# Kernel optimization log

Hardware: AMD Instinct MI355X
Metric: run time of the kernel (lower is better)

The kernel has to match this reference:

```python
import jax, jax.numpy as jnp
import numpy as np

K = 20          # knn neighbors (init kwarg k)
LEAK = 0.2      # LeakyReLU negative slope
EPS = 1e-5      # BatchNorm eps


def knn(x, k):
    # x: (B, D, N) -> indices (B, N, K) of k nearest (largest negative sq-dist)
    inner = -2.0 * jnp.einsum('bin,bim->bnm', x, x)
    xx = jnp.sum(x * x, axis=1, keepdims=True)            # (B,1,N)
    pd = -xx - inner - jnp.swapaxes(xx, 1, 2)             # (B,N,N)
    return jax.lax.top_k(pd, k)[1]


def gather_graph_feature(x, idx):
    # x: (B,D,N), idx: (B,N,K) -> (B, 2D, N, K)
    feat = jax.vmap(lambda xb, ib: xb[:, ib])(x, idx)     # (B,D,N,K)
    xc = x[..., None]                                     # (B,D,N,1)
    return jnp.concatenate([feat - xc, jnp.broadcast_to(xc, feat.shape)], axis=1)


def bn_lrelu(y, g, b, axes):
    mu = jnp.mean(y, axis=axes, keepdims=True)
    var = jnp.var(y, axis=axes, keepdims=True)            # biased var (torch BN train)
    shape = [1] * y.ndim
    shape[1] = -1
    y = (y - mu) * jax.lax.rsqrt(var + EPS) * g.reshape(shape) + b.reshape(shape)
    return jnp.where(y >= 0, y, LEAK * y)


def edge_block(x, idx, w, g, b):
    f = gather_graph_feature(x, idx)                      # (B,2D,N,K)
    y = jnp.einsum('oc,bcnk->bonk', w, f)                 # 1x1 Conv2d, no bias
    y = bn_lrelu(y, g, b, (0, 2, 3))
    return jnp.max(y, axis=-1)                            # max over K -> (B,O,N)


def setup_inputs() -> dict:
    key = jax.random.key(0)
    ks = jax.random.split(key, 8)
    B, D, N = 2, 2, 4096
    out_dim = 512
    pts = jax.random.normal(ks[0], (B, D, N), dtype=jnp.float32)
    dims = [(64, 4), (64, 128), (128, 128), (256, 256), (out_dim, 512)]
    inp = {'pts': pts}
    for i, (o, c) in enumerate(dims):
        inp[f'w{i+1}'] = jax.random.normal(ks[i + 1], (o, c), dtype=jnp.float32) * 0.05
        inp[f'g{i+1}'] = jnp.ones((o,), dtype=jnp.float32)
        inp[f'b{i+1}'] = jnp.zeros((o,), dtype=jnp.float32)
    return inp


def reference(pts, w1, g1, b1, w2, g2, b2, w3, g3, b3, w4, g4, b4, w5, g5, b5):
    idx = knn(pts, K)
    x1 = edge_block(pts, idx, w1, g1, b1)   # (B,64,N)
    x2 = edge_block(x1, idx, w2, g2, b2)    # (B,64,N)
    x3 = edge_block(x2, idx, w3, g3, b3)    # (B,128,N)
    x4 = edge_block(x3, idx, w4, g4, b4)    # (B,256,N)
    x = jnp.concatenate([x1, x2, x3, x4], axis=1)         # (B,512,N)
    y = jnp.einsum('oc,bcn->bon', w5, x)                  # 1x1 Conv1d, no bias
    return bn_lrelu(y, g5, b5, (0, 2))
```

## Files before the change

### kernel.cpp

```cpp
#include <hip/hip_runtime.h>
#include <hip/hip_bf16.h>
#include <math.h>

#define BB 2
#define NN 4096
#define PP (BB*NN)
#define KK 20
#define LEAK 0.2f
#define EPSB 1e-5f

typedef short sv8 __attribute__((ext_vector_type(8)));
typedef float f4  __attribute__((ext_vector_type(4)));

__device__ inline unsigned short f2bf(float f) {
    unsigned u = __float_as_uint(f);
    unsigned r = (u + 0x7FFFu + ((u >> 16) & 1u)) >> 16;
    return (unsigned short)r;
}
__device__ inline float bf2f(unsigned short h) {
    return __uint_as_float((unsigned)h << 16);
}
__device__ inline void gload16(const void* g, void* l) {
    __builtin_amdgcn_global_load_lds(
        (const __attribute__((address_space(1))) unsigned int*)g,
        (__attribute__((address_space(3))) unsigned int*)l, 16, 0, 0);
}

__global__ __launch_bounds__(256) void knn_kernel(const float* __restrict__ pts,
                                                  int* __restrict__ idx,
                                                  float* __restrict__ pts_t) {
    __shared__ unsigned int hist[256];
    __shared__ unsigned int scanres[3];
    __shared__ unsigned int cnt2[2];
    __shared__ unsigned long long blist[512];

    int r = blockIdx.x;
    int b = r >> 12, n = r & (NN - 1);
    const float* X0 = pts + (size_t)b * 2 * NN;
    const float* X1 = X0 + NN;
    int tid = threadIdx.x;
    float x0n = X0[n], x1n = X1[n];
    if (tid == 0) {
        pts_t[(size_t)r * 2 + 0] = x0n;
        pts_t[(size_t)r * 2 + 1] = x1n;
    }
    float xxn = __fadd_rn(__fmul_rn(x0n, x0n), __fmul_rn(x1n, x1n));
    float negxxn = __fsub_rn(0.f, xxn);

    float pdv[16];
    #pragma unroll
    for (int q = 0; q < 16; ++q) {
        int m = q * 256 + tid;
        float x0m = X0[m], x1m = X1[m];
        float xxm = __fadd_rn(__fmul_rn(x0m, x0m), __fmul_rn(x1m, x1m));
        float dot = __builtin_fmaf(x1n, x1m, __fmul_rn(x0n, x0m));
        float inner = __fmul_rn(-2.f, dot);
        float t1 = __fsub_rn(negxxn, inner);
        pdv[q] = __fsub_rn(t1, xxm);
    }

    int shift = 24;
    for (int attempt = 0; attempt < 3; ++attempt) {
        hist[tid] = 0;
        __syncthreads();
        float scale = (float)(1u << shift);
        #pragma unroll
        for (int q = 0; q < 16; ++q) {
            float s = fmaxf(-pdv[q], 0.f);
            unsigned int ki = (unsigned int)fminf(s * scale, 4.294e9f);
            unsigned int bin = ki >> 16;
            if (bin < 255u) atomicAdd(&hist[bin], 1u);
        }
        __syncthreads();
        if (tid < 64) {
            uint4 hv = *(const uint4*)&hist[tid * 4];
            unsigned int p0 = hv.x, p1 = p0 + hv.y, p2 = p1 + hv.z, p3 = p2 + hv.w;
            unsigned int lanesum = p3, inc = p3;
            #pragma unroll
            for (int s2 = 1; s2 < 64; s2 <<= 1) {
                unsigned int o = __shfl_up(inc, s2, 64);
                if (tid >= s2) inc += o;
            }
            unsigned int excl = inc - lanesum;
            bool flag = (inc >= KK);
            unsigned long long bal = __ballot(flag);
            int firstlane = (bal == 0ULL) ? -1 : (__ffsll((long long)bal) - 1);
            if (tid == 0) scanres[0] = (bal != 0ULL) ? 1u : 0u;
            if (tid == firstlane) {
                unsigned int c0 = excl + p0, c1 = excl + p1, c2 = excl + p2;
                int t = (c0 >= KK) ? 0 : (c1 >= KK) ? 1 : (c2 >= KK) ? 2 : 3;
                unsigned int cumb = (t == 0) ? excl : (t == 1) ? c0 : (t == 2) ? c1 : c2;
                scanres[1] = (unsigned)(tid * 4 + t);
                scanres[2] = cumb;
            }
        }
        __syncthreads();
        if (scanres[0]) break;
        shift -= 6;
        __syncthreads();
    }

    unsigned int bstar = scanres[1];
    unsigned int cumb  = scanres[2];
    if (tid == 0) { cnt2[0] = 0; cnt2[1] = 0; }
    __syncthreads();

    float scale = (float)(1u << shift);
    #pragma unroll
    for (int q = 0; q < 16; ++q) {
        float s = fmaxf(-pdv[q], 0.f);
        unsigned int ki = (unsigned int)fminf(s * scale, 4.294e9f);
        unsigned int bin = ki >> 16;
        if (bin > 255u) bin = 255u;
        int m = q * 256 + tid;
        if (bin < bstar) {
            unsigned int slot = atomicAdd(&cnt2[0], 1u);
            idx[(size_t)r * KK + slot] = m;
        } else if (bin == bstar) {
            unsigned int pos = atomicAdd(&cnt2[1], 1u);
            if (pos < 512u) {
                unsigned int ub = __float_as_uint(pdv[q]);
                unsigned int fk = (ub & 0x80000000u) ? ~ub : (ub | 0x80000000u);
                blist[pos] = ((unsigned long long)(~fk) << 32) | (unsigned int)m;
            }
        }
    }
    __syncthreads();

    int need = KK - (int)cumb;
    int L = (int)min(cnt2[1], 512u);
    if (tid < 64) {
        unsigned long long e[8];
        #pragma unroll
        for (int i = 0; i < 8; ++i) {
            int p = tid + 64 * i;
            e[i] = (p < L) ? blist[p] : ~0ULL;
        }
        unsigned long long lmin = e[0];
        #pragma unroll
        for (int i = 1; i < 8; ++i) lmin = (e[i] < lmin) ? e[i] : lmin;
        for (int p = 0; p < need; ++p) {
            unsigned long long gm = lmin;
            #pragma unroll
            for (int s2 = 32; s2 > 0; s2 >>= 1) {
                unsigned long long o = __shfl_xor(gm, s2, 64);
                if (o < gm) gm = o;
            }
            if (lmin == gm) {
                #pragma unroll
                for (int i = 0; i < 8; ++i) if (e[i] == gm) e[i] = ~0ULL;
                lmin = e[0];
                #pragma unroll
                for (int i = 1; i < 8; ++i) lmin = (e[i] < lmin) ? e[i] : lmin;
                idx[(size_t)r * KK + cumb + p] = (int)(gm & 0xFFFFFFFFu);
            }
        }
    }
}

__global__ __launch_bounds__(256) void proj_gemm(const float* __restrict__ X, int ldx, int C,
                                                 const float* __restrict__ W, int O, int mode,
                                                 float* __restrict__ outU, float* __restrict__ outV) {
    __shared__ float Xs[16][65];
    __shared__ float Ws[16][65];
    int row0 = blockIdx.x * 64, col0 = blockIdx.y * 64;
    int tid = threadIdx.x;
    int tx = tid % 16, ty = tid / 16;
    float acc[4][4] = {};
    for (int c0 = 0; c0 < C; c0 += 16) {
        for (int i = 0; i < 4; ++i) {
            int mm = ty + i * 16;
            float val = 0.f;
            if (c0 + tx < C) val = X[(size_t)(row0 + mm) * ldx + c0 + tx];
            Xs[tx][mm] = val;
        }
        for (int i = 0; i < 4; ++i) {
            int jj = ty + i * 16;
            int j = col0 + jj;
            float val = 0.f;
            if (c0 + tx < C) {
                if (mode == 0) {
                    if (j < O) val = W[(size_t)j * (2 * C) + c0 + tx];
                    else {
                        const float* wr = W + (size_t)(j - O) * (2 * C);
                        val = wr[C + c0 + tx] - wr[c0 + tx];
                    }
                } else {
                    val = W[(size_t)j * C + c0 + tx];
                }
            }
            Ws[tx][jj] = val;
        }
        __syncthreads();
        int kmax = (C - c0 < 16) ? (C - c0) : 16;
        for (int kk = 0; kk < kmax; ++kk) {
            float a[4], bw[4];
            #pragma unroll
            for (int i = 0; i < 4; ++i) a[i] = Xs[kk][ty * 4 + i];
            #pragma unroll
            for (int j = 0; j < 4; ++j) bw[j] = Ws[kk][tx * 4 + j];
            #pragma unroll
            for (int i = 0; i < 4; ++i)
                #pragma unroll
                for (int j = 0; j < 4; ++j)
                    acc[i][j] = fmaf(a[i], bw[j], acc[i][j]);
        }
        __syncthreads();
    }
    for (int i = 0; i < 4; ++i) {
        int rr = row0 + ty * 4 + i;
        for (int j = 0; j < 4; ++j) {
            int jg = col0 + tx * 4 + j;
            float vv = acc[i][j];
            if (mode == 0) {
                if (jg < O) outU[(size_t)rr * O + jg] = vv;
                else        outV[(size_t)rr * O + (jg - O)] = vv;
            } else {
                outU[(size_t)rr * O + jg] = vv;
            }
        }
    }
}

__global__ __launch_bounds__(256) void convert_all(const float* __restrict__ w2,
                                                   const float* __restrict__ w3,
                                                   const float* __restrict__ w4,
                                                   const float* __restrict__ w5,
                                                   unsigned short* __restrict__ bh,
                                                   unsigned short* __restrict__ bl) {
    int i = blockIdx.x * 256 + threadIdx.x;
    if (i >= 352256) return;
    const float* w; int O, C, mode, base;
    if (i < 8192)       { w = w2; O = 64;  C = 64;  mode = 0; base = 0; }
    else if (i < 24576) { w = w3; O = 128; C = 64;  mode = 0; base = 8192; }
    else if (i < 90112) { w = w4; O = 256; C = 128; mode = 0; base = 24576; }
    else                { w = w5; O = 512; C = 512; mode = 1; base = 90112; }
    int j = i - base;
    int row = j / C, c = j - row * C;
    float v;
    if (mode == 0) {
        if (row < O) v = w[(size_t)row * 2 * C + c];
        else {
            const float* wr = w + (size_t)(row - O) * 2 * C;
            v = wr[C + c] - wr[c];
        }
    } else {
        v = w[(size_t)row * C + c];
    }
    unsigned short h = f2bf(v);
    bh[i] = h;
    bl[i] = f2bf(v - bf2f(h));
}

__global__ __launch_bounds__(256) void mfma_gemm64(const unsigned short* __restrict__ Xh,
                                                   const unsigned short* __restrict__ Xl,
                                                   int ldx, int K,
                                                   const unsigned short* __restrict__ Bh,
                                                   const unsigned short* __restrict__ Bl,
                                                   int O,
                                                   float* __restrict__ outU,
                                                   float* __restrict__ outV) {
    __shared__ unsigned short Ah[256 * 8], Al[256 * 8], Bhs[256 * 8], Bls[256 * 8];
    int row0 = blockIdx.x * 64, col0 = blockIdx.y * 64;
    int tid = threadIdx.x;
    int wid = tid >> 6, lane = tid & 63;
    int wm = wid & 1, wn = wid >> 1;
    int l15 = lane & 15, l4 = lane >> 4;
    int m = tid & 63, kb = tid >> 6;

    f4 acc[2][2];
    #pragma unroll
    for (int i = 0; i < 2; ++i)
        #pragma unroll
        for (int j = 0; j < 2; ++j) { acc[i][j][0]=0.f; acc[i][j][1]=0.f; acc[i][j][2]=0.f; acc[i][j][3]=0.f; }

    for (int k0 = 0; k0 < K; k0 += 32) {
        size_t ga = (size_t)(row0 + m) * ldx + k0 + kb * 8;
        size_t gb = (size_t)(col0 + m) * K + k0 + kb * 8;
        gload16(Xh + ga, &Ah[(size_t)(wid * 64) * 8]);
        gload16(Xl + ga, &Al[(size_t)(wid * 64) * 8]);
        gload16(Bh + gb, &Bhs[(size_t)(wid * 64) * 8]);
        gload16(Bl + gb, &Bls[(size_t)(wid * 64) * 8]);
        __syncthreads();

        sv8 bhf[2], blf[2];
        #pragma unroll
        for (int fn = 0; fn < 2; ++fn) {
            int nn2 = wn * 32 + fn * 16 + l15;
            bhf[fn] = *(const sv8*)&Bhs[(size_t)(l4 * 64 + nn2) * 8];
            blf[fn] = *(const sv8*)&Bls[(size_t)(l4 * 64 + nn2) * 8];
        }
        #pragma unroll
        for (int fm = 0; fm < 2; ++fm) {
            int mm = wm * 32 + fm * 16 + l15;
            sv8 ah = *(const sv8*)&Ah[(size_t)(l4 * 64 + mm) * 8];
            sv8 al = *(const sv8*)&Al[(size_t)(l4 * 64 + mm) * 8];
            #pragma unroll
            for (int fn = 0; fn < 2; ++fn) {
                acc[fm][fn] = __builtin_amdgcn_mfma_f32_16x16x32_bf16(ah, bhf[fn], acc[fm][fn], 0, 0, 0);
                acc[fm][fn] = __builtin_amdgcn_mfma_f32_16x16x32_bf16(ah, blf[fn], acc[fm][fn], 0, 0, 0);
                acc[fm][fn] = __builtin_amdgcn_mfma_f32_16x16x32_bf16(al, bhf[fn], acc[fm][fn], 0, 0, 0);
            }
        }
        __syncthreads();
    }

    #pragma unroll
    for (int fm = 0; fm < 2; ++fm) {
        int rbase = row0 + wm * 32 + fm * 16 + l4 * 4;
        #pragma unroll
        for (int fn = 0; fn < 2; ++fn) {
            int jg = col0 + wn * 32 + fn * 16 + l15;
            #pragma unroll
            for (int e = 0; e < 4; ++e) {
                float vv = acc[fm][fn][e];
                int p = rbase + e;
                if (jg < O) outU[(size_t)p * O + jg] = vv;
                else        outV[(size_t)p * O + (jg - O)] = vv;
            }
        }
    }
}

__global__ __launch_bounds__(256) void mfma_gemm128s(const unsigned short* __restrict__ Xh,
                                                     int ldx, int K,
                                                     const unsigned short* __restrict__ Bh,
                                                     int O,
                                                     float* __restrict__ outU) {
    __shared__ unsigned short Ah[512 * 8], Bhs[512 * 8];
    int row0 = blockIdx.x * 128, col0 = blockIdx.y * 128;
    int tid = threadIdx.x;
    int wid = tid >> 6, lane = tid & 63;
    int wm = wid & 1, wn = wid >> 1;
    int l15 = lane & 15, l4 = lane >> 4;

    f4 acc[4][4];
    #pragma unroll
    for (int i = 0; i < 4; ++i)
        #pragma unroll
        for (int j = 0; j < 4; ++j) { acc[i][j][0]=0.f; acc[i][j][1]=0.f; acc[i][j][2]=0.f; acc[i][j][3]=0.f; }

    for (int k0 = 0; k0 < K; k0 += 32) {
        #pragma unroll
        for (int j = 0; j < 2; ++j) {
            int c = tid + 256 * j;
            int m = c & 127, kb = c >> 7;
            size_t ga = (size_t)(row0 + m) * ldx + k0 + kb * 8;
            size_t gb = (size_t)(col0 + m) * K + k0 + kb * 8;
            gload16(Xh + ga, &Ah[(size_t)(wid * 64 + 256 * j) * 8]);
            gload16(Bh + gb, &Bhs[(size_t)(wid * 64 + 256 * j) * 8]);
        }
        __syncthreads();

        sv8 bhf[4];
        #pragma unroll
        for (int fn = 0; fn < 4; ++fn) {
            int nn2 = wn * 64 + fn * 16 + l15;
            bhf[fn] = *(const sv8*)&Bhs[(size_t)(l4 * 128 + nn2) * 8];
        }
        #pragma unroll
        for (int fm = 0; fm < 4; ++fm) {
            int mm = wm * 64 + fm * 16 + l15;
            sv8 ah = *(const sv8*)&Ah[(size_t)(l4 * 128 + mm) * 8];
            #pragma unroll
            for (int fn = 0; fn < 4; ++fn)
                acc[fm][fn] = __builtin_amdgcn_mfma_f32_16x16x32_bf16(ah, bhf[fn], acc[fm][fn], 0, 0, 0);
        }
        __syncthreads();
    }

    #pragma unroll
    for (int fm = 0; fm < 4; ++fm) {
        int rbase = row0 + wm * 64 + fm * 16 + l4 * 4;
        #pragma unroll
        for (int fn = 0; fn < 4; ++fn) {
            int jg = col0 + wn * 64 + fn * 16 + l15;
            #pragma unroll
            for (int e = 0; e < 4; ++e)
                outU[(size_t)(rbase + e) * O + jg] = acc[fm][fn][e];
        }
    }
}

__global__ __launch_bounds__(256) void edge_stats(const float* __restrict__ u,
                                                  const float* __restrict__ v,
                                                  const int* __restrict__ idx,
                                                  int O, int PPL,
                                                  float* __restrict__ mx, float* __restrict__ mn,
                                                  float* __restrict__ partial) {
    __shared__ float red[4 * 256];
    int tid = threadIdx.x;
    int CH2 = O >> 1;
    int PS = 256 / CH2;
    int co = tid % CH2;
    int ps = tid / CH2;
    float s1a = 0.f, s1b = 0.f, s2a = 0.f, s2b = 0.f;
    for (int pi = 0; pi < PPL; ++pi) {
        int r = (blockIdx.x * PS + ps) * PPL + pi;
        int b = r >> 12;
        const float* ub = u + (size_t)b * NN * O + 2 * co;
        float2 vv = *(const float2*)&v[(size_t)r * O + 2 * co];
        const int* ip = idx + (size_t)r * KK;
        int mreg[KK];
        #pragma unroll
        for (int k = 0; k < KK; ++k) mreg[k] = ip[k];
        float2 uv[KK];
        #pragma unroll
        for (int k = 0; k < KK; ++k) uv[k] = *(const float2*)&ub[(size_t)mreg[k] * O];
        float bxa = -INFINITY, bxb = -INFINITY, bna = INFINITY, bnb = INFINITY;
        #pragma unroll
        for (int k = 0; k < KK; ++k) {
            float y0 = uv[k].x + vv.x, y1 = uv[k].y + vv.y;
            s1a += y0; s2a = fmaf(y0, y0, s2a);
            s1b += y1; s2b = fmaf(y1, y1, s2b);
            bxa = fmaxf(bxa, y0); bna = fminf(bna, y0);
            bxb = fmaxf(bxb, y1); bnb = fminf(bnb, y1);
        }
        *(float2*)&mx[(size_t)r * O + 2 * co] = make_float2(bxa, bxb);
        *(float2*)&mn[(size_t)r * O + 2 * co] = make_float2(bna, bnb);
    }
    red[0 * 256 + tid] = s1a;
    red[1 * 256 + tid] = s1b;
    red[2 * 256 + tid] = s2a;
    red[3 * 256 + tid] = s2b;
    __syncthreads();
    for (int s = PS >> 1; s > 0; s >>= 1) {
        if (ps < s) {
            int oth = tid + s * CH2;
            red[0 * 256 + tid] += red[0 * 256 + oth];
            red[1 * 256 + tid] += red[1 * 256 + oth];
            red[2 * 256 + tid] += red[2 * 256 + oth];
            red[3 * 256 + tid] += red[3 * 256 + oth];
        }
        __syncthreads();
    }
    if (ps == 0) {
        size_t base = (size_t)blockIdx.x * 2 * O;
        partial[base + 2 * co]         = red[0 * 256 + tid];
        partial[base + 2 * co + 1]     = red[1 * 256 + tid];
        partial[base + O + 2 * co]     = red[2 * 256 + tid];
        partial[base + O + 2 * co + 1] = red[3 * 256 + tid];
    }
}

__global__ __launch_bounds__(256) void stats_reduce(const float* __restrict__ partial, int nblk,
                                                    int O, float cnt,
                                                    const float* __restrict__ g,
                                                    const float* __restrict__ bsh,
                                                    float* __restrict__ st) {
    __shared__ float r1[4], r2[4];
    int o = blockIdx.x, tid = threadIdx.x;
    float s1 = 0.f, s2 = 0.f;
    for (int bk = tid; bk < nblk; bk += 256) {
        size_t base = (size_t)bk * 2 * O;
        s1 += partial[base + o];
        s2 += partial[base + O + o];
    }
    #pragma unroll
    for (int s = 32; s > 0; s >>= 1) {
        s1 += __shfl_down(s1, s, 64);
        s2 += __shfl_down(s2, s, 64);
    }
    if ((tid & 63) == 0) { r1[tid >> 6] = s1; r2[tid >> 6] = s2; }
    __syncthreads();
    if (tid == 0) {
        s1 = r1[0] + r1[1] + r1[2] + r1[3];
        s2 = r2[0] + r2[1] + r2[2] + r2[3];
        float mu = s1 / cnt;
        float var = s2 / cnt - mu * mu;
        float x = var + EPSB;
        float rr = rsqrtf(x);
        rr = rr * (1.5f - 0.5f * x * rr * rr);
        float sc = g[o] * rr;
        st[o] = sc;
        st[O + o] = bsh[o] - mu * sc;
    }
}

__global__ void apply_edge(const float* __restrict__ mx, const float* __restrict__ mn,
                           const float* __restrict__ st, int O, int choff,
                           unsigned short* __restrict__ xh, unsigned short* __restrict__ xl,
                           int writelo) {
    int e2 = blockIdx.x * 256 + threadIdx.x;
    int half = O >> 1;
    if (e2 >= PP * half) return;
    int r = e2 / half, o = (e2 - r * half) * 2;
    float2 sc = *(const float2*)&st[o];
    float2 tt = *(const float2*)&st[O + o];
    float2 vx = *(const float2*)&mx[(size_t)r * O + o];
    float2 vn = *(const float2*)&mn[(size_t)r * O + o];
    float b0 = (sc.x >= 0.f) ? vx.x : vn.x;
    float b1 = (sc.y >= 0.f) ? vx.y : vn.y;
    float y0 = fmaf(sc.x, b0, tt.x); y0 = (y0 >= 0.f) ? y0 : LEAK * y0;
    float y1 = fmaf(sc.y, b1, tt.y); y1 = (y1 >= 0.f) ? y1 : LEAK * y1;
    unsigned short h0 = f2bf(y0), h1 = f2bf(y1);
    size_t d = (size_t)r * 512 + choff + o;
    ((unsigned int*)xh)[d >> 1] = (unsigned int)h0 | ((unsigned int)h1 << 16);
    if (writelo) {
        unsigned short l0 = f2bf(y0 - bf2f(h0)), l1 = f2bf(y1 - bf2f(h1));
        ((unsigned int*)xl)[d >> 1] = (unsigned int)l0 | ((unsigned int)l1 << 16);
    }
}

__global__ __launch_bounds__(256) void final_stats(const float* __restrict__ y5,
                                                   float* __restrict__ partial) {
    int blk = blockIdx.x, t = threadIdx.x;
    float s1a = 0.f, s2a = 0.f, s1b = 0.f, s2b = 0.f;
    for (int rr = 0; rr < 128; ++rr) {
        size_t row = (size_t)(blk * 128 + rr) * 512;
        float va = y5[row + t], vb = y5[row + t + 256];
        s1a += va; s2a = fmaf(va, va, s2a);
        s1b += vb; s2b = fmaf(vb, vb, s2b);
    }
    partial[((size_t)blk * 512 + t) * 2 + 0] = s1a;
    partial[((size_t)blk * 512 + t) * 2 + 1] = s2a;
    partial[((size_t)blk * 512 + t + 256) * 2 + 0] = s1b;
    partial[((size_t)blk * 512 + t + 256) * 2 + 1] = s2b;
}

__global__ __launch_bounds__(64) void final_reduce(const float* __restrict__ partial, int nblk,
                                                   float cnt,
                                                   const float* __restrict__ g,
                                                   const float* __restrict__ bsh,
                                                   float* __restrict__ st) {
    int c = blockIdx.x, tid = threadIdx.x;
    float s1 = 0.f, s2 = 0.f;
    for (int bk = tid; bk < nblk; bk += 64) {
        size_t base = ((size_t)bk * 512 + c) * 2;
        s1 += partial[base];
        s2 += partial[base + 1];
    }
    #pragma unroll
    for (int s = 32; s > 0; s >>= 1) {
        s1 += __shfl_down(s1, s, 64);
        s2 += __shfl_down(s2, s, 64);
    }
    if (tid == 0) {
        float mu = s1 / cnt;
        float var = s2 / cnt - mu * mu;
        float x = var + EPSB;
        float rr = rsqrtf(x);
        rr = rr * (1.5f - 0.5f * x * rr * rr);
        float sc = g[c] * rr;
        st[c] = sc;
        st[512 + c] = bsh[c] - mu * sc;
    }
}

__global__ __launch_bounds__(256) void final_apply(const float* __restrict__ y5,
                                                   const float* __restrict__ st,
                                                   float* __restrict__ out) {
    __shared__ float tile[32][33];
    int n0 = blockIdx.x * 32, o0 = blockIdx.y * 32, b = blockIdx.z;
    int tx = threadIdx.x, ty = threadIdx.y;
    for (int i = 0; i < 4; ++i) {
        int nl = ty + i * 8;
        tile[nl][tx] = y5[((size_t)(b * NN + n0 + nl)) * 512 + o0 + tx];
    }
    __syncthreads();
    for (int i = 0; i < 4; ++i) {
        int ol = ty + i * 8;
        int o = o0 + ol;
        float sc = st[o], tt = st[512 + o];
        float yv = fmaf(sc, tile[tx][ol], tt);
        yv = (yv >= 0.f) ? yv : LEAK * yv;
        out[((size_t)b * 512 + o) * NN + n0 + tx] = yv;
    }
}

extern "C" void kernel_launch(void* const* d_in, const int* in_sizes, int n_in,
                              void* d_out, int out_size, void* d_ws, size_t ws_size,
                              hipStream_t stream) {
    const float* pts = (const float*)d_in[0];
    const float* w[5]; const float* g[5]; const float* bsh[5];
    for (int i = 0; i < 5; ++i) {
        w[i]   = (const float*)d_in[1 + 3 * i];
        g[i]   = (const float*)d_in[2 + 3 * i];
        bsh[i] = (const float*)d_in[3 + 3 * i];
    }
    float* out = (float*)d_out;

    unsigned short* xh = (unsigned short*)d_ws;
    unsigned short* xl = xh + (size_t)PP * 512;
    float* u    = (float*)(xl + (size_t)PP * 512);
    float* v    = u    + (size_t)PP * 256;
    float* mxb  = v    + (size_t)PP * 256;
    float* mnb  = mxb  + (size_t)PP * 256;
    float* y5   = u;
    float* ptst = mnb  + (size_t)PP * 256;
    int*   idxb = (int*)(ptst + (size_t)PP * 2);
    float* part = (float*)(idxb + (size_t)PP * KK);
    float* st   = part + (size_t)1048576;
    unsigned short* wh_all = (unsigned short*)(st + 1024);
    unsigned short* wl_all = wh_all + 352256;

    knn_kernel<<<PP, 256, 0, stream>>>(pts, idxb, ptst);
    convert_all<<<1376, 256, 0, stream>>>(w[1], w[2], w[3], w[4], wh_all, wl_all);

    const int Cs[4]    = {2, 64, 64, 128};
    const int Os[4]    = {64, 64, 128, 256};
    const int choffs[4]= {0, 64, 128, 256};
    const int inoffs[4]= {0, 0, 64, 128};
    const int woffs[4] = {0, 0, 8192, 24576};

    for (int li = 0; li < 4; ++li) {
        int C = Cs[li], O = Os[li];
        if (li == 0) {
            dim3 gg(PP / 64, (2 * O) / 64);
            proj_gemm<<<gg, 256, 0, stream>>>(ptst, 2, C, w[0], O, 0, u, v);
        } else {
            dim3 gg(PP / 64, (2 * O) / 64);
            mfma_gemm64<<<gg, 256, 0, stream>>>(xh + inoffs[li], xl + inoffs[li], 512, C,
                                                wh_all + woffs[li], wl_all + woffs[li], O, u, v);
        }
        int PS  = 512 / O;
        int PPL = (O == 256) ? 2 : 1;
        int nblk = PP / (PS * PPL);
        edge_stats<<<nblk, 256, 0, stream>>>(u, v, idxb, O, PPL, mxb, mnb, part);
        stats_reduce<<<O, 256, 0, stream>>>(part, nblk, O, (float)((size_t)PP * KK),
                                            g[li], bsh[li], st);
        apply_edge<<<(PP * O / 2 + 255) / 256, 256, 0, stream>>>(
            mxb, mnb, st, O, choffs[li], xh, xl, (li == 3) ? 0 : 1);
    }

    dim3 gf(PP / 128, 512 / 128);
    mfma_gemm128s<<<gf, 256, 0, stream>>>(xh, 512, 512, wh_all + 90112, 512, y5);
    final_stats<<<64, 256, 0, stream>>>(y5, part);
    final_reduce<<<512, 64, 0, stream>>>(part, 64, (float)PP, g[4], bsh[4], st);
    final_apply<<<dim3(NN / 32, 512 / 32, BB), dim3(32, 8), 0, stream>>>(y5, st, out);
}
```

Before: 194.0 us.

## Fuse final BN stats into GEMM epilogue, specialize layer-1 projection, cache kNN bins

The final GEMM now reduces per-column sum and sum of squares in its epilogue and writes one partial per row block, so the separate final_stats pass over y5 goes away and final_reduce reads 64 partials directly. The generic tiled proj_gemm for layer 1 is replaced by an elementwise kernel that reads points directly, which also drops the transposed points copy from the kNN kernel. The kNN kernel keeps its computed bin indices in registers instead of recomputing them in the selection pass, at the cost of extra register pressure.

```diff
diff --git a/kernel.cpp b/kernel.cpp
--- a/kernel.cpp
+++ b/kernel.cpp
@@ -27,8 +27,7 @@
 }
 
 __global__ __launch_bounds__(256) void knn_kernel(const float* __restrict__ pts,
-                                                  int* __restrict__ idx,
-                                                  float* __restrict__ pts_t) {
+                                                  int* __restrict__ idx) {
     __shared__ unsigned int hist[256];
     __shared__ unsigned int scanres[3];
     __shared__ unsigned int cnt2[2];
@@ -40,10 +39,6 @@
     const float* X1 = X0 + NN;
     int tid = threadIdx.x;
     float x0n = X0[n], x1n = X1[n];
-    if (tid == 0) {
-        pts_t[(size_t)r * 2 + 0] = x0n;
-        pts_t[(size_t)r * 2 + 1] = x1n;
-    }
     float xxn = __fadd_rn(__fmul_rn(x0n, x0n), __fmul_rn(x1n, x1n));
     float negxxn = __fsub_rn(0.f, xxn);
 
@@ -59,6 +54,7 @@
         pdv[q] = __fsub_rn(t1, xxm);
     }
 
+    int bins[16];
     int shift = 24;
     for (int attempt = 0; attempt < 3; ++attempt) {
         hist[tid] = 0;
@@ -69,6 +65,8 @@
             float s = fmaxf(-pdv[q], 0.f);
             unsigned int ki = (unsigned int)fminf(s * scale, 4.294e9f);
             unsigned int bin = ki >> 16;
+            if (bin > 255u) bin = 255u;
+            bins[q] = (int)bin;
             if (bin < 255u) atomicAdd(&hist[bin], 1u);
         }
         __syncthreads();
@@ -100,18 +98,14 @@
         __syncthreads();
     }
 
-    unsigned int bstar = scanres[1];
-    unsigned int cumb  = scanres[2];
+    int bstar = (int)scanres[1];
+    unsigned int cumb = scanres[2];
     if (tid == 0) { cnt2[0] = 0; cnt2[1] = 0; }
     __syncthreads();
 
-    float scale = (float)(1u << shift);
     #pragma unroll
     for (int q = 0; q < 16; ++q) {
-        float s = fmaxf(-pdv[q], 0.f);
-        unsigned int ki = (unsigned int)fminf(s * scale, 4.294e9f);
-        unsigned int bin = ki >> 16;
-        if (bin > 255u) bin = 255u;
+        int bin = bins[q];
         int m = q * 256 + tid;
         if (bin < bstar) {
             unsigned int slot = atomicAdd(&cnt2[0], 1u);
@@ -158,68 +152,18 @@
     }
 }
 
-__global__ __launch_bounds__(256) void proj_gemm(const float* __restrict__ X, int ldx, int C,
-                                                 const float* __restrict__ W, int O, int mode,
-                                                 float* __restrict__ outU, float* __restrict__ outV) {
-    __shared__ float Xs[16][65];
-    __shared__ float Ws[16][65];
-    int row0 = blockIdx.x * 64, col0 = blockIdx.y * 64;
-    int tid = threadIdx.x;
-    int tx = tid % 16, ty = tid / 16;
-    float acc[4][4] = {};
-    for (int c0 = 0; c0 < C; c0 += 16) {
-        for (int i = 0; i < 4; ++i) {
-            int mm = ty + i * 16;
-            float val = 0.f;
-            if (c0 + tx < C) val = X[(size_t)(row0 + mm) * ldx + c0 + tx];
-            Xs[tx][mm] = val;
-        }
-        for (int i = 0; i < 4; ++i) {
-            int jj = ty + i * 16;
-            int j = col0 + jj;
-            float val = 0.f;
-            if (c0 + tx < C) {
-                if (mode == 0) {
-                    if (j < O) val = W[(size_t)j * (2 * C) + c0 + tx];
-                    else {
-                        const float* wr = W + (size_t)(j - O) * (2 * C);
-                        val = wr[C + c0 + tx] - wr[c0 + tx];
-                    }
-                } else {
-                    val = W[(size_t)j * C + c0 + tx];
-                }
-            }
-            Ws[tx][jj] = val;
-        }
-        __syncthreads();
-        int kmax = (C - c0 < 16) ? (C - c0) : 16;
-        for (int kk = 0; kk < kmax; ++kk) {
-            float a[4], bw[4];
-            #pragma unroll
-            for (int i = 0; i < 4; ++i) a[i] = Xs[kk][ty * 4 + i];
-            #pragma unroll
-            for (int j = 0; j < 4; ++j) bw[j] = Ws[kk][tx * 4 + j];
-            #pragma unroll
-            for (int i = 0; i < 4; ++i)
-                #pragma unroll
-                for (int j = 0; j < 4; ++j)
-                    acc[i][j] = fmaf(a[i], bw[j], acc[i][j]);
-        }
-        __syncthreads();
-    }
-    for (int i = 0; i < 4; ++i) {
-        int rr = row0 + ty * 4 + i;
-        for (int j = 0; j < 4; ++j) {
-            int jg = col0 + tx * 4 + j;
-            float vv = acc[i][j];
-            if (mode == 0) {
-                if (jg < O) outU[(size_t)rr * O + jg] = vv;
-                else        outV[(size_t)rr * O + (jg - O)] = vv;
-            } else {
-                outU[(size_t)rr * O + jg] = vv;
-            }
-        }
-    }
+__global__ __launch_bounds__(256) void l1_proj(const float* __restrict__ pts,
+                                               const float* __restrict__ w1,
+                                               float* __restrict__ u,
+                                               float* __restrict__ v) {
+    int e = blockIdx.x * 256 + threadIdx.x;
+    int r = e >> 6, o = e & 63;
+    int b = r >> 12, n = r & (NN - 1);
+    float x0 = pts[(size_t)b * 2 * NN + n];
+    float x1 = pts[(size_t)b * 2 * NN + NN + n];
+    float4 wr = *(const float4*)&w1[(size_t)o * 4];
+    u[(size_t)r * 64 + o] = fmaf(wr.x, x0, wr.y * x1);
+    v[(size_t)r * 64 + o] = fmaf(wr.z - wr.x, x0, (wr.w - wr.y) * x1);
 }
 
 __global__ __launch_bounds__(256) void convert_all(const float* __restrict__ w2,
@@ -326,8 +270,10 @@
                                                      int ldx, int K,
                                                      const unsigned short* __restrict__ Bh,
                                                      int O,
-                                                     float* __restrict__ outU) {
+                                                     float* __restrict__ outU,
+                                                     float* __restrict__ partial) {
     __shared__ unsigned short Ah[512 * 8], Bhs[512 * 8];
+    __shared__ float sred1[2][128], sred2[2][128];
     int row0 = blockIdx.x * 128, col0 = blockIdx.y * 128;
     int tid = threadIdx.x;
     int wid = tid >> 6, lane = tid & 63;
@@ -379,6 +325,30 @@
             for (int e = 0; e < 4; ++e)
                 outU[(size_t)(rbase + e) * O + jg] = acc[fm][fn][e];
         }
+    }
+
+    #pragma unroll
+    for (int fn = 0; fn < 4; ++fn) {
+        float a1 = 0.f, a2 = 0.f;
+        #pragma unroll
+        for (int fm = 0; fm < 4; ++fm)
+            #pragma unroll
+            for (int e = 0; e < 4; ++e) { float t = acc[fm][fn][e]; a1 += t; a2 = fmaf(t, t, a2); }
+        a1 += __shfl_xor(a1, 16, 64); a2 += __shfl_xor(a2, 16, 64);
+        a1 += __shfl_xor(a1, 32, 64); a2 += __shfl_xor(a2, 32, 64);
+        if (lane < 16) {
+            int cb = wn * 64 + fn * 16 + lane;
+            sred1[wm][cb] = a1;
+            sred2[wm][cb] = a2;
+        }
+    }
+    __syncthreads();
+    if (tid < 128) {
+        float s1 = sred1[0][tid] + sred1[1][tid];
+        float s2 = sred2[0][tid] + sred2[1][tid];
+        size_t pbase = (size_t)blockIdx.x * 1024 + (size_t)(col0 + tid) * 2;
+        partial[pbase]     = s1;
+        partial[pbase + 1] = s2;
     }
 }
 
@@ -502,34 +472,14 @@
     }
 }
 
-__global__ __launch_bounds__(256) void final_stats(const float* __restrict__ y5,
-                                                   float* __restrict__ partial) {
-    int blk = blockIdx.x, t = threadIdx.x;
-    float s1a = 0.f, s2a = 0.f, s1b = 0.f, s2b = 0.f;
-    for (int rr = 0; rr < 128; ++rr) {
-        size_t row = (size_t)(blk * 128 + rr) * 512;
-        float va = y5[row + t], vb = y5[row + t + 256];
-        s1a += va; s2a = fmaf(va, va, s2a);
-        s1b += vb; s2b = fmaf(vb, vb, s2b);
-    }
-    partial[((size_t)blk * 512 + t) * 2 + 0] = s1a;
-    partial[((size_t)blk * 512 + t) * 2 + 1] = s2a;
-    partial[((size_t)blk * 512 + t + 256) * 2 + 0] = s1b;
-    partial[((size_t)blk * 512 + t + 256) * 2 + 1] = s2b;
-}
-
-__global__ __launch_bounds__(64) void final_reduce(const float* __restrict__ partial, int nblk,
+__global__ __launch_bounds__(64) void final_reduce(const float* __restrict__ partial,
                                                    float cnt,
                                                    const float* __restrict__ g,
                                                    const float* __restrict__ bsh,
                                                    float* __restrict__ st) {
     int c = blockIdx.x, tid = threadIdx.x;
-    float s1 = 0.f, s2 = 0.f;
-    for (int bk = tid; bk < nblk; bk += 64) {
-        size_t base = ((size_t)bk * 512 + c) * 2;
-        s1 += partial[base];
-        s2 += partial[base + 1];
-    }
+    size_t base = (size_t)tid * 1024 + (size_t)c * 2;
+    float s1 = partial[base], s2 = partial[base + 1];
     #pragma unroll
     for (int s = 32; s > 0; s >>= 1) {
         s1 += __shfl_down(s1, s, 64);
@@ -594,7 +544,7 @@
     unsigned short* wh_all = (unsigned short*)(st + 1024);
     unsigned short* wl_all = wh_all + 352256;
 
-    knn_kernel<<<PP, 256, 0, stream>>>(pts, idxb, ptst);
+    knn_kernel<<<PP, 256, 0, stream>>>(pts, idxb);
     convert_all<<<1376, 256, 0, stream>>>(w[1], w[2], w[3], w[4], wh_all, wl_all);
 
     const int Cs[4]    = {2, 64, 64, 128};
@@ -606,8 +556,7 @@
     for (int li = 0; li < 4; ++li) {
         int C = Cs[li], O = Os[li];
         if (li == 0) {
-            dim3 gg(PP / 64, (2 * O) / 64);
-            proj_gemm<<<gg, 256, 0, stream>>>(ptst, 2, C, w[0], O, 0, u, v);
+            l1_proj<<<PP * 64 / 256, 256, 0, stream>>>(pts, w[0], u, v);
         } else {
             dim3 gg(PP / 64, (2 * O) / 64);
             mfma_gemm64<<<gg, 256, 0, stream>>>(xh + inoffs[li], xl + inoffs[li], 512, C,
@@ -624,8 +573,7 @@
     }
 
     dim3 gf(PP / 128, 512 / 128);
-    mfma_gemm128s<<<gf, 256, 0, stream>>>(xh, 512, 512, wh_all + 90112, 512, y5);
-    final_stats<<<64, 256, 0, stream>>>(y5, part);
-    final_reduce<<<512, 64, 0, stream>>>(part, 64, (float)PP, g[4], bsh[4], st);
+    mfma_gemm128s<<<gf, 256, 0, stream>>>(xh, 512, 512, wh_all + 90112, 512, y5, part);
+    final_reduce<<<512, 64, 0, stream>>>(part, (float)PP, g[4], bsh[4], st);
     final_apply<<<dim3(NN / 32, 512 / 32, BB), dim3(32, 8), 0, stream>>>(y5, st, out);
 }
```

Measured after the change: 186.6 us. -3.8%, faster.
